# Kernel optimization log

Hardware: AMD Instinct MI355X
Metric: run time of the kernel (lower is better)

The kernel has to match this reference:

```python
import jax, jax.numpy as jnp
import numpy as np

B, T, D, R = 4, 2048, 1024, 64  # batch, seq_len, hidden_dim, max_relative_position


def setup_inputs() -> dict:
    key = jax.random.key(0)
    ks = jax.random.split(key, 11)
    s = 1.0 / np.sqrt(D)

    def lin(k):
        return (jax.random.normal(k, (D, D), jnp.float32) * s)

    return {
        "repre": jax.random.normal(ks[0], (B, T, D), jnp.float32),
        "mask": jnp.ones((B, T, T), jnp.int32),  # 1 = valid position
        "st_Wq": lin(ks[1]), "st_bq": jnp.zeros((D,), jnp.float32),
        "st_Wk": lin(ks[2]), "st_bk": jnp.zeros((D,), jnp.float32),
        "st_rel": jax.random.normal(ks[3], (2 * R + 1, D), jnp.float32) * 0.02,
        "ed_Wq": lin(ks[4]), "ed_bq": jnp.zeros((D,), jnp.float32),
        "ed_Wk": lin(ks[5]), "ed_bk": jnp.zeros((D,), jnp.float32),
        "ed_rel": jax.random.normal(ks[6], (2 * R + 1, D), jnp.float32) * 0.02,
    }


def _attn_logits(x, Wq, bq, Wk, bk, rel, mask):
    # Single-head attention scores with relative-position key bias (OpenNMT style).
    d = x.shape[-1]
    q = (x @ Wq + bq) * (1.0 / jnp.sqrt(jnp.float32(d)))  # [B,T,D], pre-scaled query
    k = x @ Wk + bk                                        # [B,T,D]
    scores = jnp.einsum('btd,bsd->bts', q, k)              # [B,T,T] content scores
    Tn = x.shape[1]
    Rn = (rel.shape[0] - 1) // 2
    pos = jnp.arange(Tn)
    # relative position matrix: clip(j - i, -R, R) + R  -> [T,T] indices
    idx = jnp.clip(pos[None, :] - pos[:, None], -Rn, Rn) + Rn
    # q . rel_emb for every relative offset, then gather per (i,j):
    # equivalent to einsum('btd,tsd->bts', q, rel[idx]) without the [T,T,D] gather.
    qr = jnp.einsum('btd,rd->btr', q, rel)                 # [B,T,2R+1]
    scores = scores + qr[:, pos[:, None], idx]             # [B,T,T]
    return jnp.where(mask.astype(bool), scores, jnp.float32(-1e18))


def reference(repre, mask, st_Wq, st_bq, st_Wk, st_bk, st_rel,
              ed_Wq, ed_bq, ed_Wk, ed_bk, ed_rel):
    span_st_logits = _attn_logits(repre, st_Wq, st_bq, st_Wk, st_bk, st_rel, mask)
    span_ed_logits = _attn_logits(repre, ed_Wq, ed_bq, ed_Wk, ed_bk, ed_rel, mask)
    return (span_st_logits, span_ed_logits)
```

## Files before the change

### kernel.cpp

```cpp
#include <hip/hip_runtime.h>

constexpr int Bn = 4;
constexpr int Tn = 2048;
constexpr int Dn = 1024;
constexpr int Rn = 64;
constexpr int RELP = 256;
constexpr int QR_STRIDE = 132;

typedef __bf16 bf8 __attribute__((ext_vector_type(8)));
typedef float f32x4 __attribute__((ext_vector_type(4)));

__device__ __forceinline__ unsigned short f2bf(float f) {
    unsigned int u = __float_as_uint(f);
    u += 0x7fffu + ((u >> 16) & 1u);
    return (unsigned short)(u >> 16);
}

#define GLDS(g, l)                                                            \
    __builtin_amdgcn_global_load_lds(                                         \
        (const __attribute__((address_space(1))) void*)(g),                   \
        (__attribute__((address_space(3))) void*)(l), 16, 0, 0)

#define MFMA_BF16(a, b, c) __builtin_amdgcn_mfma_f32_16x16x32_bf16(a, b, c, 0, 0, 0)

__device__ __forceinline__ void mfma_gemm_256_k32(
    const unsigned short* __restrict__ Ab,
    const unsigned short* __restrict__ Bb,
    f32x4 (&acc)[8][4], unsigned short* As, unsigned short* Bs)
{
    const int tid  = threadIdx.x;
    const int lane = tid & 63, wid = tid >> 6;
    const int wr = wid >> 2, wc = wid & 3;
    const int l15 = lane & 15, lq = lane >> 4;

    const int pc = (((l15 & 1) << 2) | lq) ^ ((l15 >> 1) & 7);
    const int lane_off = ((l15 >> 1) << 6) + (pc << 3);
    const int aoff = wr * 4096 + lane_off;
    const int boff = wc * 2048 + lane_off;

    const int P0 = tid, P1 = tid + 512;
    const int cr0 = P0 >> 3, cr1 = P1 >> 3;
    const int c0 = cr0 * 8 + ((P0 & 7) ^ (cr0 & 7));
    const int c1 = cr1 * 8 + ((P1 & 7) ^ (cr1 & 7));
    const size_t g0 = (size_t)(c0 >> 2) * Dn + (size_t)((c0 & 3) << 3);
    const size_t g1 = (size_t)(c1 >> 2) * Dn + (size_t)((c1 & 3) << 3);
    const int d0 = P0 * 8, d1 = P1 * 8;

#define STAGE(src, buf)                                                       \
    do {                                                                      \
        GLDS((src) + g0, (buf) + d0);                                         \
        GLDS((src) + g1, (buf) + d1);                                         \
    } while (0)

    constexpr int NT = Dn / 32;

    STAGE(Ab, As);
    STAGE(Bb, Bs);
    asm volatile("s_waitcnt vmcnt(0)" ::: "memory");
    __builtin_amdgcn_s_barrier();

    bf8 a8[8], b4[4];
#pragma unroll 1
    for (int T = 0; T < NT; ++T) {
        const int cb = (T & 1) << 13;
        const int sb = cb ^ 8192;
        if (T + 1 < NT) {
            STAGE(Ab + (T + 1) * 32, As + sb);
            STAGE(Bb + (T + 1) * 32, Bs + sb);
        }
#pragma unroll
        for (int m = 0; m < 8; ++m)
            a8[m] = *(const bf8*)&As[cb + aoff + m * 512];
#pragma unroll
        for (int n = 0; n < 4; ++n)
            b4[n] = *(const bf8*)&Bs[cb + boff + n * 512];
        __builtin_amdgcn_s_setprio(1);
#pragma unroll
        for (int m = 0; m < 8; ++m)
#pragma unroll
            for (int n = 0; n < 4; ++n)
                acc[m][n] = MFMA_BF16(a8[m], b4[n], acc[m][n]);
        __builtin_amdgcn_s_setprio(0);
        __builtin_amdgcn_sched_barrier(0);
        if (T + 1 < NT)
            asm volatile("s_waitcnt vmcnt(0)" ::: "memory");
        __builtin_amdgcn_s_barrier();
    }
#undef STAGE
}

__device__ __forceinline__ void mfma_gemm_128(
    const unsigned short* __restrict__ Ab,
    const unsigned short* __restrict__ Bb,
    int K, f32x4 acc[4][4],
    unsigned short* As, unsigned short* Bs)
{
    const int tid = threadIdx.x;
    const int r0  = tid >> 2;
    const int c8  = (tid & 3) * 8;
    const int lane = tid & 63;
    const int w    = tid >> 6;
    const int wm = (w & 1) * 64, wn = (w >> 1) * 64;
    const int l15 = lane & 15, lq = lane >> 4;

    const int nt = K >> 5;

    GLDS(Ab + (size_t)r0 * K + c8,        As + r0 * 32 + c8);
    GLDS(Ab + ((size_t)r0 + 64) * K + c8, As + (r0 + 64) * 32 + c8);
    GLDS(Bb + (size_t)r0 * K + c8,        Bs + r0 * 32 + c8);
    GLDS(Bb + ((size_t)r0 + 64) * K + c8, Bs + (r0 + 64) * 32 + c8);
    __syncthreads();

    int cur = 0;
    for (int t = 0; t < nt; ++t) {
        if (t + 1 < nt) {
            const int k0 = (t + 1) << 5;
            const int nb = (cur ^ 1) * (128 * 32);
            GLDS(Ab + (size_t)r0 * K + k0 + c8,        As + nb + r0 * 32 + c8);
            GLDS(Ab + ((size_t)r0 + 64) * K + k0 + c8, As + nb + (r0 + 64) * 32 + c8);
            GLDS(Bb + (size_t)r0 * K + k0 + c8,        Bs + nb + r0 * 32 + c8);
            GLDS(Bb + ((size_t)r0 + 64) * K + k0 + c8, Bs + nb + (r0 + 64) * 32 + c8);
        }
        const int cbuf = cur * (128 * 32);
        bf8 a[4], b[4];
#pragma unroll
        for (int i = 0; i < 4; ++i) {
            a[i] = *(const bf8*)&As[cbuf + (wm + i * 16 + l15) * 32 + lq * 8];
            b[i] = *(const bf8*)&Bs[cbuf + (wn + i * 16 + l15) * 32 + lq * 8];
        }
#pragma unroll
        for (int i = 0; i < 4; ++i)
#pragma unroll
            for (int j = 0; j < 4; ++j)
                acc[i][j] = MFMA_BF16(a[i], b[j], acc[i][j]);
        __syncthreads();
        cur ^= 1;
    }
}

__global__ __launch_bounds__(256) void cvt_bf16(
    const float* __restrict__ in, unsigned short* __restrict__ out, int n4)
{
    int i = blockIdx.x * 256 + threadIdx.x;
    if (i < n4) {
        float4 v = ((const float4*)in)[i];
        ushort4 o;
        o.x = f2bf(v.x); o.y = f2bf(v.y); o.z = f2bf(v.z); o.w = f2bf(v.w);
        ((ushort4*)out)[i] = o;
    }
}

__global__ __launch_bounds__(256) void wt_transpose(
    const float* __restrict__ w0, const float* __restrict__ w1,
    const float* __restrict__ w2, const float* __restrict__ w3,
    unsigned short* __restrict__ WT)
{
    __shared__ float t[32][33];
    const int z = blockIdx.z;
    const float* W = z == 0 ? w0 : z == 1 ? w1 : z == 2 ? w2 : w3;
    const int x = blockIdx.x * 32 + threadIdx.x;
    const int y0 = blockIdx.y * 32;
#pragma unroll
    for (int j = 0; j < 32; j += 8)
        t[threadIdx.y + j][threadIdx.x] = W[(size_t)(y0 + threadIdx.y + j) * Dn + x];
    __syncthreads();
    unsigned short* o = WT + (size_t)z * Dn * Dn;
    const int n0 = blockIdx.x * 32;
#pragma unroll
    for (int j = 0; j < 32; j += 8)
        o[(size_t)(n0 + threadIdx.y + j) * Dn + y0 + threadIdx.x] =
            f2bf(t[threadIdx.x][threadIdx.y + j]);
}

__global__ __launch_bounds__(256) void rel_pad(
    const float* __restrict__ st_rel, const float* __restrict__ ed_rel,
    unsigned short* __restrict__ relb)
{
    const int z = blockIdx.y;
    const float* in = z ? ed_rel : st_rel;
    const int i4 = blockIdx.x * 256 + threadIdx.x;
    const int row = (i4 * 4) >> 10;
    const int col = (i4 * 4) & 1023;
    ushort4 o; o.x = 0; o.y = 0; o.z = 0; o.w = 0;
    if (row < 2 * Rn + 1) {
        float4 v = *(const float4*)(in + (size_t)row * 1024 + col);
        o.x = f2bf(v.x); o.y = f2bf(v.y); o.z = f2bf(v.z); o.w = f2bf(v.w);
    }
    ((ushort4*)(relb + (size_t)z * RELP * 1024))[i4] = o;
}

__global__ __launch_bounds__(256) void mask_pack(
    const int* __restrict__ mask, unsigned long long* __restrict__ pm)
{
    const int g = blockIdx.x * 256 + threadIdx.x;
    const int v = mask[g];
    unsigned long long b = __ballot(v != 0);
    if ((threadIdx.x & 63) == 0) pm[g >> 6] = b;
}

__global__ __launch_bounds__(512, 2) void proj_gemm256(
    const unsigned short* __restrict__ Xb, const unsigned short* __restrict__ Wb,
    const float* __restrict__ b0, const float* __restrict__ b1,
    const float* __restrict__ b2, const float* __restrict__ b3,
    unsigned short* __restrict__ outQK, float qscale)
{
    __shared__ unsigned short As[2 * 8192], Bs[2 * 8192];
    const int z = blockIdx.z;
    const float* bias = z == 0 ? b0 : z == 1 ? b1 : z == 2 ? b2 : b3;
    const float scale = (z & 1) ? 1.0f : qscale;

    const unsigned short* Ab = Xb + (size_t)blockIdx.x * 256 * Dn;
    const unsigned short* Bb = Wb + ((size_t)z * Dn + blockIdx.y * 256) * Dn;

    f32x4 zero = {0.f, 0.f, 0.f, 0.f};
    f32x4 acc[8][4];
#pragma unroll
    for (int i = 0; i < 8; ++i)
#pragma unroll
        for (int j = 0; j < 4; ++j) acc[i][j] = zero;

    mfma_gemm_256_k32(Ab, Bb, acc, As, Bs);

    const int tid = threadIdx.x, lane = tid & 63, wid = tid >> 6;
    const int wr = wid >> 2, wc = wid & 3;
    const int l15 = lane & 15, lq = lane >> 4;
    unsigned short* out = outQK + (size_t)z * (size_t)Bn * Tn * Dn;
    const int row0 = blockIdx.x * 256 + wr * 128 + lq * 4;
    const int col0 = blockIdx.y * 256 + wc * 64 + l15;

#pragma unroll
    for (int ni = 0; ni < 4; ++ni) {
        const int col = col0 + ni * 16;
        const float bvv = bias[col];
#pragma unroll
        for (int mi = 0; mi < 8; ++mi)
#pragma unroll
            for (int r = 0; r < 4; ++r) {
                const int row = row0 + mi * 16 + r;
                out[(size_t)row * Dn + col] = f2bf((acc[mi][ni][r] + bvv) * scale);
            }
    }
}

__global__ __launch_bounds__(256) void qr_gemm(
    const unsigned short* __restrict__ QKb, const unsigned short* __restrict__ relb,
    float* __restrict__ QR)
{
    __shared__ unsigned short As[2 * 128 * 32], Bs[2 * 128 * 32];
    const int z = blockIdx.z;
    const unsigned short* Ab = QKb + ((size_t)(z * 2) * Bn * Tn + blockIdx.x * 128) * Dn;
    const unsigned short* Bb = relb + ((size_t)z * RELP + blockIdx.y * 128) * Dn;

    f32x4 zero = {0.f, 0.f, 0.f, 0.f};
    f32x4 acc[4][4];
#pragma unroll
    for (int i = 0; i < 4; ++i)
#pragma unroll
        for (int j = 0; j < 4; ++j) acc[i][j] = zero;

    mfma_gemm_128(Ab, Bb, Dn, acc, As, Bs);

    const int tid = threadIdx.x, lane = tid & 63, w = tid >> 6;
    const int wm = (w & 1) * 64, wn = (w >> 1) * 64;
    const int l15 = lane & 15, lq = lane >> 4;
    float* out = QR + (size_t)z * (size_t)Bn * Tn * QR_STRIDE;

#pragma unroll
    for (int ni = 0; ni < 4; ++ni) {
        const int col = blockIdx.y * 128 + wn + ni * 16 + l15;
        if (col >= 2 * Rn + 1) continue;
#pragma unroll
        for (int mi = 0; mi < 4; ++mi) {
#pragma unroll
            for (int r = 0; r < 4; ++r) {
                const int row = blockIdx.x * 128 + wm + mi * 16 + lq * 4 + r;
                out[(size_t)row * QR_STRIDE + col] = acc[mi][ni][r];
            }
        }
    }
}

__global__ __launch_bounds__(512, 2) void scores_gemm256(
    const unsigned short* __restrict__ QKb, const float* __restrict__ QR,
    const unsigned int* __restrict__ pmask, float* __restrict__ Out)
{
    __shared__ unsigned short As[2 * 8192], Bs[2 * 8192];
    const int z = blockIdx.z;
    const int side = z >> 2, bt = z & 3;

    const unsigned short* Ab =
        QKb + ((size_t)side * 2 * Bn * Tn + (size_t)bt * Tn + blockIdx.x * 256) * Dn;
    const unsigned short* Bb =
        QKb + (((size_t)side * 2 + 1) * Bn * Tn + (size_t)bt * Tn + blockIdx.y * 256) * Dn;
    const float* QRb = QR + ((size_t)side * Bn * Tn + (size_t)bt * Tn) * QR_STRIDE;
    const unsigned int* pmb = pmask + (size_t)bt * Tn * (Tn / 32);
    float* outb = Out + ((size_t)side * Bn + bt) * (size_t)Tn * Tn;

    f32x4 zero = {0.f, 0.f, 0.f, 0.f};
    f32x4 acc[8][4];
#pragma unroll
    for (int i = 0; i < 8; ++i)
#pragma unroll
        for (int j = 0; j < 4; ++j) acc[i][j] = zero;

    mfma_gemm_256_k32(Ab, Bb, acc, As, Bs);

    const int tid = threadIdx.x, lane = tid & 63, wid = tid >> 6;
    const int wr = wid >> 2, wc = wid & 3;
    const int l15 = lane & 15, lq = lane >> 4;
    const int i0 = blockIdx.x * 256 + wr * 128 + lq * 4;
    const int j0 = blockIdx.y * 256 + wc * 64 + l15;

#pragma unroll
    for (int mi = 0; mi < 8; ++mi) {
#pragma unroll
        for (int r = 0; r < 4; ++r) {
            const int i = i0 + mi * 16 + r;
            const float* qrow = QRb + (size_t)i * QR_STRIDE;
            const unsigned int* mwrow = pmb + (size_t)i * (Tn / 32);
            float* orow = outb + (size_t)i * Tn;
#pragma unroll
            for (int ni = 0; ni < 4; ++ni) {
                const int j = j0 + ni * 16;
                int d = j - i;
                d = d < -Rn ? -Rn : (d > Rn ? Rn : d);
                const float qv = qrow[d + Rn];
                const unsigned int mw = mwrow[j >> 5];
                const bool ok = (mw >> (j & 31)) & 1u;
                orow[j] = ok ? acc[mi][ni][r] + qv : -1e18f;
            }
        }
    }
}

extern "C" void kernel_launch(void* const* d_in, const int* in_sizes, int n_in,
                              void* d_out, int out_size, void* d_ws, size_t ws_size,
                              hipStream_t stream) {
    const float* repre  = (const float*)d_in[0];
    const int*   mask   = (const int*)  d_in[1];
    const float* st_Wq  = (const float*)d_in[2];
    const float* st_bq  = (const float*)d_in[3];
    const float* st_Wk  = (const float*)d_in[4];
    const float* st_bk  = (const float*)d_in[5];
    const float* st_rel = (const float*)d_in[6];
    const float* ed_Wq  = (const float*)d_in[7];
    const float* ed_bq  = (const float*)d_in[8];
    const float* ed_Wk  = (const float*)d_in[9];
    const float* ed_bk  = (const float*)d_in[10];
    const float* ed_rel = (const float*)d_in[11];
    float* out = (float*)d_out;

    const size_t MT = (size_t)Bn * Tn;

    unsigned short* Xb   = (unsigned short*)d_ws;
    unsigned short* Wb   = Xb + MT * Dn;
    unsigned short* relb = Wb + (size_t)4 * Dn * Dn;
    unsigned short* QKb  = relb + (size_t)2 * RELP * Dn;
    float* QRbuf = (float*)(QKb + (size_t)4 * MT * Dn);
    unsigned long long* pmask = (unsigned long long*)Xb;

    const float qscale = 0.03125f;
    dim3 blk(256);

    {
        int n4 = (int)(MT * Dn / 4);
        cvt_bf16<<<dim3((n4 + 255) / 256), blk, 0, stream>>>(repre, Xb, n4);
        wt_transpose<<<dim3(32, 32, 4), dim3(32, 8), 0, stream>>>(
            st_Wq, st_Wk, ed_Wq, ed_Wk, Wb);
        rel_pad<<<dim3(RELP * Dn / 4 / 256, 2), blk, 0, stream>>>(st_rel, ed_rel, relb);
    }

    proj_gemm256<<<dim3((int)MT / 256, Dn / 256, 4), dim3(512), 0, stream>>>(
        Xb, Wb, st_bq, st_bk, ed_bq, ed_bk, QKb, qscale);

    mask_pack<<<dim3((int)(Bn * (size_t)Tn * Tn / 256)), blk, 0, stream>>>(
        mask, pmask);

    qr_gemm<<<dim3((int)MT / 128, RELP / 128, 2), blk, 0, stream>>>(QKb, relb, QRbuf);

    scores_gemm256<<<dim3(Tn / 256, Tn / 256, 8), dim3(512), 0, stream>>>(
        QKb, QRbuf, (const unsigned int*)pmask, out);
}
```

Measured before the change: 535.9 us.

## Rewrite 256x256 GEMM mainloop with BK=64 interleaved staging and XCD-aware block mapping

Replaces the K=32 double-buffered GEMM mainloop with a BK=64 scheme. Global-to-LDS loads for the next tile are issued in halves and interleaved between four MFMA sub-blocks, separated by explicit barriers and partial vmcnt waits. Both the projection and scores kernels now use a 1D grid remapped so blocks that share inputs land on the same XCD, aiming for better L2 reuse. LDS usage doubles to 128KB per block, which may lower occupancy, and the many extra barriers add sync overhead.

```diff
diff --git a/kernel.cpp b/kernel.cpp
--- a/kernel.cpp
+++ b/kernel.cpp
@@ -23,7 +23,51 @@
 
 #define MFMA_BF16(a, b, c) __builtin_amdgcn_mfma_f32_16x16x32_bf16(a, b, c, 0, 0, 0)
 
-__device__ __forceinline__ void mfma_gemm_256_k32(
+#define PRE_MFMA()                                                            \
+    do {                                                                      \
+        __builtin_amdgcn_sched_barrier(0);                                    \
+        __builtin_amdgcn_s_barrier();                                         \
+        asm volatile("s_waitcnt lgkmcnt(0)" ::: "memory");                    \
+        __builtin_amdgcn_sched_barrier(0);                                    \
+    } while (0)
+#define POST_MFMA()                                                           \
+    do {                                                                      \
+        __builtin_amdgcn_sched_barrier(0);                                    \
+        __builtin_amdgcn_s_barrier();                                         \
+    } while (0)
+
+__device__ __forceinline__ void rd_a4(bf8 (&a)[4][2], const unsigned short* As,
+                                      int base, int mb, int ck0, int ck1) {
+#pragma unroll
+    for (int m = 0; m < 4; ++m) {
+        a[m][0] = *(const bf8*)&As[base + (mb + m) * 1024 + ck0];
+        a[m][1] = *(const bf8*)&As[base + (mb + m) * 1024 + ck1];
+    }
+}
+__device__ __forceinline__ void rd_b2(bf8 (&b)[2][2], const unsigned short* Bs,
+                                      int base, int nb, int ck0, int ck1) {
+#pragma unroll
+    for (int n = 0; n < 2; ++n) {
+        b[n][0] = *(const bf8*)&Bs[base + (nb + n) * 1024 + ck0];
+        b[n][1] = *(const bf8*)&Bs[base + (nb + n) * 1024 + ck1];
+    }
+}
+__device__ __forceinline__ void mm8(f32x4 (&acc)[8][4], const bf8 (&a)[4][2],
+                                    const bf8 (&b)[2][2], int mb, int nb) {
+    __builtin_amdgcn_s_setprio(1);
+#pragma unroll
+    for (int m = 0; m < 4; ++m)
+#pragma unroll
+        for (int n = 0; n < 2; ++n) {
+            f32x4 c = acc[mb + m][nb + n];
+            c = MFMA_BF16(a[m][0], b[n][0], c);
+            c = MFMA_BF16(a[m][1], b[n][1], c);
+            acc[mb + m][nb + n] = c;
+        }
+    __builtin_amdgcn_s_setprio(0);
+}
+
+__device__ __forceinline__ void mfma_gemm_256_bk64(
     const unsigned short* __restrict__ Ab,
     const unsigned short* __restrict__ Bb,
     f32x4 (&acc)[8][4], unsigned short* As, unsigned short* Bs)
@@ -32,61 +76,78 @@
     const int lane = tid & 63, wid = tid >> 6;
     const int wr = wid >> 2, wc = wid & 3;
     const int l15 = lane & 15, lq = lane >> 4;
-
-    const int pc = (((l15 & 1) << 2) | lq) ^ ((l15 >> 1) & 7);
-    const int lane_off = ((l15 >> 1) << 6) + (pc << 3);
-    const int aoff = wr * 4096 + lane_off;
-    const int boff = wc * 2048 + lane_off;
-
-    const int P0 = tid, P1 = tid + 512;
-    const int cr0 = P0 >> 3, cr1 = P1 >> 3;
-    const int c0 = cr0 * 8 + ((P0 & 7) ^ (cr0 & 7));
-    const int c1 = cr1 * 8 + ((P1 & 7) ^ (cr1 & 7));
-    const size_t g0 = (size_t)(c0 >> 2) * Dn + (size_t)((c0 & 3) << 3);
-    const size_t g1 = (size_t)(c1 >> 2) * Dn + (size_t)((c1 & 3) << 3);
-    const int d0 = P0 * 8, d1 = P1 * 8;
-
-#define STAGE(src, buf)                                                       \
+    const int ax  = l15 & 7;
+    const int ck0 = (lq ^ ax) << 3;
+    const int ck1 = ((4 | lq) ^ ax) << 3;
+    const int abase = wr * 8192 + l15 * 64;
+    const int bbase = (wc >> 1) * 8192 + (wc & 1) * 4096 + l15 * 64;
+
+    const int prow = tid >> 3;
+    const int scol = ((tid & 7) ^ (prow & 7)) << 3;
+    const int g0 = prow * Dn + scol;
+    const int g1 = (prow + 64) * Dn + scol;
+    const int d0 = tid * 8, d1 = tid * 8 + 4096;
+
+#define STG_A(t, h, dstoff)                                                   \
     do {                                                                      \
-        GLDS((src) + g0, (buf) + d0);                                         \
-        GLDS((src) + g1, (buf) + d1);                                         \
+        const unsigned short* s_ = Ab + (size_t)(h) * 128 * Dn + (t) * 64;    \
+        GLDS(s_ + g0, As + (dstoff) + d0);                                    \
+        GLDS(s_ + g1, As + (dstoff) + d1);                                    \
     } while (0)
-
-    constexpr int NT = Dn / 32;
-
-    STAGE(Ab, As);
-    STAGE(Bb, Bs);
-    asm volatile("s_waitcnt vmcnt(0)" ::: "memory");
+#define STG_B(t, h, dstoff)                                                   \
+    do {                                                                      \
+        const unsigned short* s_ = Bb + (size_t)(h) * 128 * Dn + (t) * 64;    \
+        GLDS(s_ + g0, Bs + (dstoff) + d0);                                    \
+        GLDS(s_ + g1, Bs + (dstoff) + d1);                                    \
+    } while (0)
+
+    STG_A(0, 0, 0); STG_A(0, 1, 8192);
+    STG_B(0, 0, 0); STG_B(0, 1, 8192);
+    STG_A(1, 0, 16384);
+    asm volatile("s_waitcnt vmcnt(2)" ::: "memory");
     __builtin_amdgcn_s_barrier();
 
-    bf8 a8[8], b4[4];
+    bf8 a[4][2], b[2][2];
 #pragma unroll 1
-    for (int T = 0; T < NT; ++T) {
-        const int cb = (T & 1) << 13;
-        const int sb = cb ^ 8192;
-        if (T + 1 < NT) {
-            STAGE(Ab + (T + 1) * 32, As + sb);
-            STAGE(Bb + (T + 1) * 32, Bs + sb);
-        }
-#pragma unroll
-        for (int m = 0; m < 8; ++m)
-            a8[m] = *(const bf8*)&As[cb + aoff + m * 512];
-#pragma unroll
-        for (int n = 0; n < 4; ++n)
-            b4[n] = *(const bf8*)&Bs[cb + boff + n * 512];
-        __builtin_amdgcn_s_setprio(1);
-#pragma unroll
-        for (int m = 0; m < 8; ++m)
-#pragma unroll
-            for (int n = 0; n < 4; ++n)
-                acc[m][n] = MFMA_BF16(a8[m], b4[n], acc[m][n]);
-        __builtin_amdgcn_s_setprio(0);
+    for (int j = 0; j < 8; ++j) {
+        const bool st = j < 7;
+        const int t0 = 2 * j;
+        rd_a4(a, As, abase, 0, ck0, ck1);
+        rd_b2(b, Bs, bbase, 0, ck0, ck1);
+        STG_A(t0 + 1, 1, 16384 + 8192);
+        PRE_MFMA(); mm8(acc, a, b, 0, 0); POST_MFMA();
+        rd_b2(b, Bs, bbase, 2, ck0, ck1);
+        STG_B(t0 + 1, 0, 16384);
+        PRE_MFMA(); mm8(acc, a, b, 0, 2); POST_MFMA();
+        rd_a4(a, As, abase, 4, ck0, ck1);
+        STG_B(t0 + 1, 1, 16384 + 8192);
+        PRE_MFMA(); mm8(acc, a, b, 4, 2); POST_MFMA();
+        rd_b2(b, Bs, bbase, 0, ck0, ck1);
+        if (st) STG_A(t0 + 2, 0, 0);
+        PRE_MFMA(); mm8(acc, a, b, 4, 0);
         __builtin_amdgcn_sched_barrier(0);
-        if (T + 1 < NT)
-            asm volatile("s_waitcnt vmcnt(0)" ::: "memory");
+        if (st) asm volatile("s_waitcnt vmcnt(2)" ::: "memory");
+        else    asm volatile("s_waitcnt vmcnt(0)" ::: "memory");
         __builtin_amdgcn_s_barrier();
-    }
-#undef STAGE
+        rd_a4(a, As, 16384 + abase, 0, ck0, ck1);
+        rd_b2(b, Bs, 16384 + bbase, 0, ck0, ck1);
+        if (st) STG_A(t0 + 2, 1, 8192);
+        PRE_MFMA(); mm8(acc, a, b, 0, 0); POST_MFMA();
+        rd_b2(b, Bs, 16384 + bbase, 2, ck0, ck1);
+        if (st) STG_B(t0 + 2, 0, 0);
+        PRE_MFMA(); mm8(acc, a, b, 0, 2); POST_MFMA();
+        rd_a4(a, As, 16384 + abase, 4, ck0, ck1);
+        if (st) STG_B(t0 + 2, 1, 8192);
+        PRE_MFMA(); mm8(acc, a, b, 4, 2); POST_MFMA();
+        rd_b2(b, Bs, 16384 + bbase, 0, ck0, ck1);
+        if (st) STG_A(t0 + 3, 0, 16384);
+        PRE_MFMA(); mm8(acc, a, b, 4, 0);
+        __builtin_amdgcn_sched_barrier(0);
+        if (st) asm volatile("s_waitcnt vmcnt(2)" ::: "memory");
+        __builtin_amdgcn_s_barrier();
+    }
+#undef STG_A
+#undef STG_B
 }
 
 __device__ __forceinline__ void mfma_gemm_128(
@@ -204,29 +265,34 @@
     const float* __restrict__ b2, const float* __restrict__ b3,
     unsigned short* __restrict__ outQK, float qscale)
 {
-    __shared__ unsigned short As[2 * 8192], Bs[2 * 8192];
-    const int z = blockIdx.z;
+    __shared__ unsigned short As[2 * 16384], Bs[2 * 16384];
+    const int bid = blockIdx.x;
+    const int xcd = bid & 7, i = bid >> 3;
+    const int p = xcd * 2 + (i >> 5);
+    const int bx = i & 31;
+    const int by = p & 3;
+    const int z  = p >> 2;
     const float* bias = z == 0 ? b0 : z == 1 ? b1 : z == 2 ? b2 : b3;
     const float scale = (z & 1) ? 1.0f : qscale;
 
-    const unsigned short* Ab = Xb + (size_t)blockIdx.x * 256 * Dn;
-    const unsigned short* Bb = Wb + ((size_t)z * Dn + blockIdx.y * 256) * Dn;
+    const unsigned short* Ab = Xb + (size_t)bx * 256 * Dn;
+    const unsigned short* Bb = Wb + ((size_t)z * Dn + by * 256) * Dn;
 
     f32x4 zero = {0.f, 0.f, 0.f, 0.f};
     f32x4 acc[8][4];
 #pragma unroll
-    for (int i = 0; i < 8; ++i)
-#pragma unroll
-        for (int j = 0; j < 4; ++j) acc[i][j] = zero;
-
-    mfma_gemm_256_k32(Ab, Bb, acc, As, Bs);
+    for (int q = 0; q < 8; ++q)
+#pragma unroll
+        for (int r = 0; r < 4; ++r) acc[q][r] = zero;
+
+    mfma_gemm_256_bk64(Ab, Bb, acc, As, Bs);
 
     const int tid = threadIdx.x, lane = tid & 63, wid = tid >> 6;
     const int wr = wid >> 2, wc = wid & 3;
     const int l15 = lane & 15, lq = lane >> 4;
     unsigned short* out = outQK + (size_t)z * (size_t)Bn * Tn * Dn;
-    const int row0 = blockIdx.x * 256 + wr * 128 + lq * 4;
-    const int col0 = blockIdx.y * 256 + wc * 64 + l15;
+    const int row0 = bx * 256 + wr * 128 + lq * 4;
+    const int col0 = by * 256 + wc * 64 + l15;
 
 #pragma unroll
     for (int ni = 0; ni < 4; ++ni) {
@@ -284,14 +350,17 @@
     const unsigned short* __restrict__ QKb, const float* __restrict__ QR,
     const unsigned int* __restrict__ pmask, float* __restrict__ Out)
 {
-    __shared__ unsigned short As[2 * 8192], Bs[2 * 8192];
-    const int z = blockIdx.z;
+    __shared__ unsigned short As[2 * 16384], Bs[2 * 16384];
+    const int bid = blockIdx.x;
+    const int z  = bid & 7;
+    const int r8 = bid >> 3;
+    const int bx = r8 & 7, by = r8 >> 3;
     const int side = z >> 2, bt = z & 3;
 
     const unsigned short* Ab =
-        QKb + ((size_t)side * 2 * Bn * Tn + (size_t)bt * Tn + blockIdx.x * 256) * Dn;
+        QKb + ((size_t)side * 2 * Bn * Tn + (size_t)bt * Tn + bx * 256) * Dn;
     const unsigned short* Bb =
-        QKb + (((size_t)side * 2 + 1) * Bn * Tn + (size_t)bt * Tn + blockIdx.y * 256) * Dn;
+        QKb + (((size_t)side * 2 + 1) * Bn * Tn + (size_t)bt * Tn + by * 256) * Dn;
     const float* QRb = QR + ((size_t)side * Bn * Tn + (size_t)bt * Tn) * QR_STRIDE;
     const unsigned int* pmb = pmask + (size_t)bt * Tn * (Tn / 32);
     float* outb = Out + ((size_t)side * Bn + bt) * (size_t)Tn * Tn;
@@ -299,17 +368,17 @@
     f32x4 zero = {0.f, 0.f, 0.f, 0.f};
     f32x4 acc[8][4];
 #pragma unroll
-    for (int i = 0; i < 8; ++i)
-#pragma unroll
-        for (int j = 0; j < 4; ++j) acc[i][j] = zero;
-
-    mfma_gemm_256_k32(Ab, Bb, acc, As, Bs);
+    for (int q = 0; q < 8; ++q)
+#pragma unroll
+        for (int r = 0; r < 4; ++r) acc[q][r] = zero;
+
+    mfma_gemm_256_bk64(Ab, Bb, acc, As, Bs);
 
     const int tid = threadIdx.x, lane = tid & 63, wid = tid >> 6;
     const int wr = wid >> 2, wc = wid & 3;
     const int l15 = lane & 15, lq = lane >> 4;
-    const int i0 = blockIdx.x * 256 + wr * 128 + lq * 4;
-    const int j0 = blockIdx.y * 256 + wc * 64 + l15;
+    const int i0 = bx * 256 + wr * 128 + lq * 4;
+    const int j0 = by * 256 + wc * 64 + l15;
 
 #pragma unroll
     for (int mi = 0; mi < 8; ++mi) {
@@ -370,7 +439,7 @@
         rel_pad<<<dim3(RELP * Dn / 4 / 256, 2), blk, 0, stream>>>(st_rel, ed_rel, relb);
     }
 
-    proj_gemm256<<<dim3((int)MT / 256, Dn / 256, 4), dim3(512), 0, stream>>>(
+    proj_gemm256<<<dim3(512), dim3(512), 0, stream>>>(
         Xb, Wb, st_bq, st_bk, ed_bq, ed_bk, QKb, qscale);
 
     mask_pack<<<dim3((int)(Bn * (size_t)Tn * Tn / 256)), blk, 0, stream>>>(
@@ -378,6 +447,6 @@
 
     qr_gemm<<<dim3((int)MT / 128, RELP / 128, 2), blk, 0, stream>>>(QKb, relb, QRbuf);
 
-    scores_gemm256<<<dim3(Tn / 256, Tn / 256, 8), dim3(512), 0, stream>>>(
+    scores_gemm256<<<dim3(512), dim3(512), 0, stream>>>(
         QKb, QRbuf, (const unsigned int*)pmask, out);
 }
```

After: 518.8 us. 1.03x faster.
